# Kernel tuning notes

Measured on AMD Instinct MI355X. Metric: run time of the kernel, lower is better.

## Reference

```python
import jax, jax.numpy as jnp
import numpy as np

N, E, R = 50000, 500000, 3
IN, HID, OUT = 128, 128, 128
NEG_SLOPE = 0.2


def setup_inputs() -> dict:
    key = jax.random.key(0)
    ks = jax.random.split(key, 16)
    g = lambda i, shape: jax.random.normal(ks[i], shape, jnp.float32) * 0.1
    return {
        "x": jax.random.normal(ks[0], (N, IN), jnp.float32),
        "edge_index": jax.random.randint(ks[1], (2, E), 0, N, jnp.int32),
        "edge_type": jax.random.randint(ks[2], (E,), 0, R, jnp.int32),
        "edge_attr": jax.random.normal(ks[3], (E, 1), jnp.float32),
        # conv1 params (RGATConv: per-relation weight, q/k/e attention vectors, edge lin, bias)
        "w1": g(4, (R, IN, HID)), "q1": g(5, (HID, 1)), "k1": g(6, (HID, 1)),
        "le1": g(7, (1, HID)), "e1": g(8, (HID, 1)), "b1": jnp.zeros((HID,), jnp.float32),
        # conv2 params
        "w2": g(9, (R, HID, OUT)), "q2": g(10, (OUT, 1)), "k2": g(11, (OUT, 1)),
        "le2": g(12, (1, OUT)), "e2": g(13, (OUT, 1)), "b2": jnp.zeros((OUT,), jnp.float32),
    }


def _rgat_conv(x, src, dst, edge_type, edge_attr, w, q, k, le, e, b):
    """PyG RGATConv: heads=1, dim=1, additive-self-attention, across-relation softmax."""
    n = x.shape[0]
    # Per-relation linear at node level (equiv. to per-edge bmm with w[edge_type])
    xw = jnp.einsum('ni,rio->rno', x, w)            # [R, N, C]
    x_j = xw[edge_type, src]                          # [E, C] transformed source feats
    x_i = xw[edge_type, dst]                          # [E, C] transformed target feats
    # additive attention logits: q(x_i) + k(x_j) + e(lin_edge(edge_attr))
    alpha = x_i @ q + x_j @ k + (edge_attr @ le) @ e  # [E, 1]
    alpha = jax.nn.leaky_relu(alpha, negative_slope=NEG_SLOPE)
    # across-relation softmax over incoming edges of each target node
    amax = jax.ops.segment_max(alpha, dst, num_segments=n)
    amax = jnp.where(jnp.isfinite(amax), amax, 0.0)   # empty segments -> 0
    ex = jnp.exp(alpha - amax[dst])
    denom = jax.ops.segment_sum(ex, dst, num_segments=n)
    alpha = ex / (denom[dst] + 1e-16)
    # weighted scatter-add aggregation, then bias (concat=True, heads=1)
    out = jax.ops.segment_sum(alpha * x_j, dst, num_segments=n)  # [N, C]
    return out + b


def reference(x, edge_index, edge_type, edge_attr,
              w1, q1, k1, le1, e1, b1,
              w2, q2, k2, le2, e2, b2):
    src, dst = edge_index[0], edge_index[1]
    h = jax.nn.relu(_rgat_conv(x, src, dst, edge_type, edge_attr, w1, q1, k1, le1, e1, b1))
    return _rgat_conv(h, src, dst, edge_type, edge_attr, w2, q2, k2, le2, e2, b2)
```

## Files before the change

kernel.cpp:

```cpp
#include <hip/hip_runtime.h>
#include <hip/hip_bf16.h>
#include <math.h>

typedef __bf16 bf16x8 __attribute__((ext_vector_type(8)));
typedef float f32x4 __attribute__((ext_vector_type(4)));

#define CDIM 128

__global__ void sentinel_kernel(float* outf) {
  if (threadIdx.x == 0) outf[0] = 12345.0f;
}

__global__ __launch_bounds__(256) void prep_kernel(
    const float* __restrict__ w1, const float* __restrict__ w2,
    __hip_bfloat16* __restrict__ wt,
    const float* __restrict__ le1, const float* __restrict__ e1,
    const float* __restrict__ le2, const float* __restrict__ e2,
    float* __restrict__ outc, int* __restrict__ deg, int perW, int n) {
  const int b = blockIdx.x;
  const int tid = threadIdx.x;
  if (b < 48) {
    int t = b * 256 + tid;
    if (t >= perW * 2) return;
    const float* w = (t < perW) ? w1 : w2;
    int tt = (t < perW) ? t : t - perW;
    int r = tt >> 11;
    int rem = tt & 2047;
    int kb = rem >> 7;
    int o = rem & 127;
    const float* wr = w + ((size_t)r << 14);
    union { __hip_bfloat16 h[8]; int4 v; } u;
#pragma unroll
    for (int j = 0; j < 8; ++j)
      u.h[j] = __float2bfloat16(wr[(size_t)(kb * 8 + j) * CDIM + o]);
    *reinterpret_cast<int4*>(wt + (size_t)t * 8) = u.v;
  } else if (b == 48) {
    __shared__ float s1[128], s2[128];
    int t = tid;
    if (t < 128) { s1[t] = le1[t] * e1[t]; s2[t] = le2[t] * e2[t]; }
    __syncthreads();
    for (int off = 64; off > 0; off >>= 1) {
      if (t < off) { s1[t] += s1[t + off]; s2[t] += s2[t + off]; }
      __syncthreads();
    }
    if (t == 0) { outc[0] = s1[0]; outc[1] = s2[0]; }
  } else {
    int i = (b - 49) * 256 + tid;
    if (i < n) deg[i] = 0;
  }
}


__global__ __launch_bounds__(256) void hist_kernel(const int* __restrict__ dstv,
                                                   int* __restrict__ deg, int E) {
  int e = blockIdx.x * 256 + threadIdx.x;
  if (e < E) atomicAdd(&deg[dstv[e]], 1);
}

__global__ __launch_bounds__(256) void scan1_kernel(const int* __restrict__ deg,
                                                    int* __restrict__ rowptr,
                                                    int* __restrict__ partials, int n) {
  __shared__ int sh[256];
  int t = threadIdx.x;
  int base = blockIdx.x * 1024;
  int idx = base + t * 4;
  int v[4]; int s = 0;
#pragma unroll
  for (int j = 0; j < 4; ++j) { v[j] = (idx + j < n) ? deg[idx + j] : 0; s += v[j]; }
  sh[t] = s;
  __syncthreads();
  for (int off = 1; off < 256; off <<= 1) {
    int x = (t >= off) ? sh[t - off] : 0;
    __syncthreads();
    sh[t] += x;
    __syncthreads();
  }
  int excl = sh[t] - s;
  if (t == 255) partials[blockIdx.x] = sh[255];
  int run = excl;
#pragma unroll
  for (int j = 0; j < 4; ++j) {
    if (idx + j < n) rowptr[idx + j] = run;
    run += v[j];
  }
}

__global__ __launch_bounds__(256) void scan2_kernel(int* __restrict__ partials, int nb) {
  __shared__ int sh[256];
  int carry = 0;
  for (int base = 0; base < nb; base += 256) {
    int i = base + threadIdx.x;
    int v = (i < nb) ? partials[i] : 0;
    sh[threadIdx.x] = v;
    __syncthreads();
    for (int off = 1; off < 256; off <<= 1) {
      int x = (threadIdx.x >= off) ? sh[threadIdx.x - off] : 0;
      __syncthreads();
      sh[threadIdx.x] += x;
      __syncthreads();
    }
    if (i < nb) partials[i] = carry + sh[threadIdx.x] - v;
    carry += sh[255];
    __syncthreads();
  }
}

__global__ __launch_bounds__(256) void scan3_kernel(int* __restrict__ rowptr,
                                                    int* __restrict__ cursor,
                                                    const int* __restrict__ partials,
                                                    int n, int E) {
  int i = blockIdx.x * 256 + threadIdx.x;
  if (i < n) {
    int v = rowptr[i] + partials[i >> 10];
    rowptr[i] = v;
    cursor[i] = v;
  } else if (i == n) {
    rowptr[n] = E;
  }
}

__global__ __launch_bounds__(256) void scatter_kernel(
    const int* __restrict__ srcv, const int* __restrict__ dstv,
    const int* __restrict__ etype, const float* __restrict__ eattr,
    int* __restrict__ cursor, int2* __restrict__ kattr, int E, int n) {
  int e = blockIdx.x * 256 + threadIdx.x;
  if (e >= E) return;
  int p = atomicAdd(&cursor[dstv[e]], 1);
  kattr[p] = make_int2(etype[e] * n + srcv[e], __float_as_int(eattr[e]));
}

__global__ __launch_bounds__(256) void gemm_xw_kernel(
    const float* __restrict__ xin, const __hip_bfloat16* __restrict__ wt,
    const float* __restrict__ qv, const float* __restrict__ kv,
    __hip_bfloat16* __restrict__ xwout, float* __restrict__ sq, float* __restrict__ sk,
    int n) {
  __shared__ __hip_bfloat16 wlds[16 * 128 * 8];
  const int r = blockIdx.y;
  const int base = blockIdx.x * 128;
  const int tid = threadIdx.x;
  {
    const int4* src = reinterpret_cast<const int4*>(wt + ((size_t)r << 14));
    int4* dst = reinterpret_cast<int4*>(wlds);
    for (int i = tid; i < 2048; i += 256) dst[i] = src[i];
  }
  __syncthreads();

  const int wave = tid >> 6, lane = tid & 63;
  const int quad = lane >> 4, c16 = lane & 15;

  bf16x8 zf;
#pragma unroll
  for (int j = 0; j < 8; ++j) zf[j] = (__bf16)0.0f;

  bf16x8 af[2][4];
#pragma unroll
  for (int h = 0; h < 2; ++h) {
    int m = base + wave * 32 + h * 16 + c16;
#pragma unroll
    for (int ks = 0; ks < 4; ++ks) {
      if (m < n) {
        const float* xp = xin + (size_t)m * CDIM + ks * 32 + quad * 8;
        f32x4 x0 = *reinterpret_cast<const f32x4*>(xp);
        f32x4 x1 = *reinterpret_cast<const f32x4*>(xp + 4);
        bf16x8 a;
#pragma unroll
        for (int j = 0; j < 4; ++j) { a[j] = (__bf16)x0[j]; a[4 + j] = (__bf16)x1[j]; }
        af[h][ks] = a;
      } else {
        af[h][ks] = zf;
      }
    }
  }

  f32x4 acc[2][8];
#pragma unroll
  for (int h = 0; h < 2; ++h)
#pragma unroll
    for (int nt = 0; nt < 8; ++nt) acc[h][nt] = (f32x4){0.f, 0.f, 0.f, 0.f};

#pragma unroll
  for (int ks = 0; ks < 4; ++ks) {
#pragma unroll
    for (int nt = 0; nt < 8; ++nt) {
      bf16x8 b = *reinterpret_cast<const bf16x8*>(
          &wlds[(((ks * 4 + quad) * 128) + nt * 16 + c16) * 8]);
      acc[0][nt] = __builtin_amdgcn_mfma_f32_16x16x32_bf16(af[0][ks], b, acc[0][nt], 0, 0, 0);
      acc[1][nt] = __builtin_amdgcn_mfma_f32_16x16x32_bf16(af[1][ks], b, acc[1][nt], 0, 0, 0);
    }
  }

  float qf[8], kf[8];
#pragma unroll
  for (int nt = 0; nt < 8; ++nt) {
    qf[nt] = qv[nt * 16 + c16];
    kf[nt] = kv[nt * 16 + c16];
  }

#pragma unroll
  for (int h = 0; h < 2; ++h) {
    int rowb = base + wave * 32 + h * 16 + quad * 4;
#pragma unroll
    for (int reg = 0; reg < 4; ++reg) {
      int grow = rowb + reg;
      float s_q = 0.f, s_k = 0.f;
#pragma unroll
      for (int nt = 0; nt < 8; ++nt) {
        float v = acc[h][nt][reg];
        if (grow < n)
          xwout[(((size_t)r * n + grow) << 7) + nt * 16 + c16] = __float2bfloat16(v);
        s_q += v * qf[nt];
        s_k += v * kf[nt];
      }
#pragma unroll
      for (int off = 1; off < 16; off <<= 1) {
        s_q += __shfl_xor(s_q, off, 64);
        s_k += __shfl_xor(s_k, off, 64);
      }
      if (c16 == 0 && grow < n) {
        sq[r * n + grow] = s_q;
        sk[r * n + grow] = s_k;
      }
    }
  }
}

__global__ __launch_bounds__(256) void aggregate_kernel(
    const int* __restrict__ rowptr, const int2* __restrict__ kattr,
    const float* __restrict__ sq, const float* __restrict__ sk,
    const __hip_bfloat16* __restrict__ xw, const float* __restrict__ bias,
    const float* __restrict__ cscal, float* __restrict__ out, int n, int do_relu) {
  const int wave = threadIdx.x >> 6, lane = threadIdx.x & 63;
  const int node = blockIdx.x * 4 + wave;
  if (node >= n) return;
  const int g = lane >> 4;
  const int sub = lane & 15;
  const float c = cscal[0];
  const int n2 = n * 2;

  const int start = rowptr[node];
  const int deg = rowptr[node + 1] - start;
  const float s0 = sq[node], s1 = sq[n + node], s2 = sq[n2 + node];

  float acc[8];
#pragma unroll
  for (int t = 0; t < 8; ++t) acc[t] = 0.f;
  float den = 0.f;

  for (int j0 = 0; j0 < deg; j0 += 4) {
    int j = j0 + g;
    if (j < deg) {
      int2 ka = kattr[start + j];
      int kk = ka.x;
      float sv = (kk >= n2) ? s2 : ((kk >= n) ? s1 : s0);
      float l = sv + sk[kk] + c * __int_as_float(ka.y);
      l = l > 0.f ? l : 0.2f * l;
      float w = __expf(l);
      bf16x8 f = *reinterpret_cast<const bf16x8*>(xw + ((size_t)kk << 7) + sub * 8);
#pragma unroll
      for (int t = 0; t < 8; ++t) acc[t] += w * (float)f[t];
      den += w;
    }
  }

#pragma unroll
  for (int t = 0; t < 8; ++t) {
    acc[t] += __shfl_xor(acc[t], 16, 64);
    acc[t] += __shfl_xor(acc[t], 32, 64);
  }
  den += __shfl_xor(den, 16, 64);
  den += __shfl_xor(den, 32, 64);

  if (g == 0) {
    float inv = 1.0f / (den + 1e-16f);
    f32x4 b0 = *reinterpret_cast<const f32x4*>(bias + sub * 8);
    f32x4 b1 = *reinterpret_cast<const f32x4*>(bias + sub * 8 + 4);
    f32x4 o0, o1;
#pragma unroll
    for (int t = 0; t < 4; ++t) {
      o0[t] = acc[t] * inv + b0[t];
      o1[t] = acc[4 + t] * inv + b1[t];
    }
    if (do_relu) {
#pragma unroll
      for (int t = 0; t < 4; ++t) {
        o0[t] = fmaxf(o0[t], 0.f);
        o1[t] = fmaxf(o1[t], 0.f);
      }
    }
    float* op = out + (size_t)node * CDIM + sub * 8;
    *reinterpret_cast<f32x4*>(op) = o0;
    *reinterpret_cast<f32x4*>(op + 4) = o1;
  }
}


extern "C" void kernel_launch(void* const* d_in, const int* in_sizes, int n_in,
                              void* d_out, int out_size, void* d_ws, size_t ws_size,
                              hipStream_t stream) {
  const float* x     = (const float*)d_in[0];
  const int*   eidx  = (const int*)d_in[1];
  const int*   etype = (const int*)d_in[2];
  const float* eattr = (const float*)d_in[3];
  const float* w1  = (const float*)d_in[4];
  const float* q1  = (const float*)d_in[5];
  const float* k1  = (const float*)d_in[6];
  const float* le1 = (const float*)d_in[7];
  const float* e1  = (const float*)d_in[8];
  const float* b1  = (const float*)d_in[9];
  const float* w2  = (const float*)d_in[10];
  const float* q2  = (const float*)d_in[11];
  const float* k2  = (const float*)d_in[12];
  const float* le2 = (const float*)d_in[13];
  const float* e2  = (const float*)d_in[14];
  const float* b2  = (const float*)d_in[15];

  const int N = in_sizes[0] / CDIM;
  const int E = in_sizes[2];
  const int R = in_sizes[4] / (CDIM * CDIM);
  const int* srcv = eidx;
  const int* dstv = eidx + E;

  char* p = (char*)d_ws;
  auto alloc = [&](size_t bytes) -> void* {
    void* q = (void*)p;
    p += (bytes + 255) & ~(size_t)255;
    return q;
  };
  float* sq       = (float*)alloc((size_t)R * N * 4);
  float* sk       = (float*)alloc((size_t)R * N * 4);
  int*   deg      = (int*)alloc((size_t)N * 4);
  int*   rowptr   = (int*)alloc((size_t)(N + 1) * 4);
  int*   cursor   = (int*)alloc((size_t)N * 4);
  int*   partials = (int*)alloc(4096);
  int2*  kattr    = (int2*)alloc((size_t)E * 8);
  __hip_bfloat16* wt = (__hip_bfloat16*)alloc((size_t)2 * R * CDIM * CDIM * 2);
  float* cscal    = (float*)alloc(256);
  __hip_bfloat16* xw = (__hip_bfloat16*)alloc((size_t)R * N * CDIM * 2);

  size_t needed = (size_t)(p - (char*)d_ws);
  if (needed > ws_size) {
    sentinel_kernel<<<1, 64, 0, stream>>>((float*)d_out);
    return;
  }

  float* outp = (float*)d_out;
  float* hbuf = outp;

  const int eg = (E + 255) / 256;
  const int nb = (N + 1023) / 1024;
  const int nodes4 = (N + 3) / 4;
  const int perW = R * 2048;
  const int prep_grid = 49 + (N + 255) / 256;

  prep_kernel<<<prep_grid, 256, 0, stream>>>(w1, w2, wt, le1, e1, le2, e2,
                                             cscal, deg, perW, N);

  hist_kernel<<<eg, 256, 0, stream>>>(dstv, deg, E);
  scan1_kernel<<<nb, 256, 0, stream>>>(deg, rowptr, partials, N);
  scan2_kernel<<<1, 256, 0, stream>>>(partials, nb);
  scan3_kernel<<<(N + 1 + 255) / 256, 256, 0, stream>>>(rowptr, cursor, partials, N, E);
  scatter_kernel<<<eg, 256, 0, stream>>>(srcv, dstv, etype, eattr, cursor, kattr, E, N);

  dim3 ggrid((N + 127) / 128, R);

  gemm_xw_kernel<<<ggrid, 256, 0, stream>>>(x, wt, q1, k1, xw, sq, sk, N);
  aggregate_kernel<<<nodes4, 256, 0, stream>>>(rowptr, kattr, sq, sk, xw, b1,
                                               cscal + 0, hbuf, N, 1);

  gemm_xw_kernel<<<ggrid, 256, 0, stream>>>(hbuf, wt + (size_t)R * CDIM * CDIM,
                                            q2, k2, xw, sq, sk, N);
  aggregate_kernel<<<nodes4, 256, 0, stream>>>(rowptr, kattr, sq, sk, xw, b2,
                                               cscal + 1, outp, N, 0);
}
```

Measured before the change: 274.5 us.

## Fuse CSR build into one cooperative kernel and loop relations inside GEMM

The six preprocessing kernels (weight convert, degree histogram, three-phase scan, scatter) are merged into a single cooperative-launch kernel separated by grid-wide syncs, removing launch gaps between them. The GEMM kernel now loops over the three relations inside each block, loading each relation's weights into LDS in turn and reusing the converted x fragments, instead of using a 2D grid with one relation per block. Risks include grid.sync overhead, a single-block partials scan that assumes nb<=256, and reduced GEMM parallelism since there are a third as many blocks.

```diff
diff --git a/kernel.cpp b/kernel.cpp
--- a/kernel.cpp
+++ b/kernel.cpp
@@ -1,6 +1,9 @@
 #include <hip/hip_runtime.h>
 #include <hip/hip_bf16.h>
+#include <hip/hip_cooperative_groups.h>
 #include <math.h>
+
+namespace cg = cooperative_groups;
 
 typedef __bf16 bf16x8 __attribute__((ext_vector_type(8)));
 typedef float f32x4 __attribute__((ext_vector_type(4)));
@@ -11,17 +14,23 @@
   if (threadIdx.x == 0) outf[0] = 12345.0f;
 }
 
-__global__ __launch_bounds__(256) void prep_kernel(
+__global__ __launch_bounds__(256) void build_kernel(
     const float* __restrict__ w1, const float* __restrict__ w2,
     __hip_bfloat16* __restrict__ wt,
     const float* __restrict__ le1, const float* __restrict__ e1,
     const float* __restrict__ le2, const float* __restrict__ e2,
-    float* __restrict__ outc, int* __restrict__ deg, int perW, int n) {
-  const int b = blockIdx.x;
-  const int tid = threadIdx.x;
-  if (b < 48) {
-    int t = b * 256 + tid;
-    if (t >= perW * 2) return;
+    float* __restrict__ cscal, int* __restrict__ deg,
+    const int* __restrict__ srcv, const int* __restrict__ dstv,
+    const int* __restrict__ etype, const float* __restrict__ eattr,
+    int* __restrict__ rowptr, int* __restrict__ cursor,
+    int* __restrict__ partials, int2* __restrict__ kattr,
+    int perW, int n, int E, int nb) {
+  cg::grid_group grid = cg::this_grid();
+  __shared__ int sh[256];
+  const int gsize = gridDim.x * 256;
+  const int gtid = blockIdx.x * 256 + threadIdx.x;
+
+  for (int t = gtid; t < perW * 2; t += gsize) {
     const float* w = (t < perW) ? w1 : w2;
     int tt = (t < perW) ? t : t - perW;
     int r = tt >> 11;
@@ -34,99 +43,81 @@
     for (int j = 0; j < 8; ++j)
       u.h[j] = __float2bfloat16(wr[(size_t)(kb * 8 + j) * CDIM + o]);
     *reinterpret_cast<int4*>(wt + (size_t)t * 8) = u.v;
-  } else if (b == 48) {
-    __shared__ float s1[128], s2[128];
-    int t = tid;
-    if (t < 128) { s1[t] = le1[t] * e1[t]; s2[t] = le2[t] * e2[t]; }
-    __syncthreads();
-    for (int off = 64; off > 0; off >>= 1) {
-      if (t < off) { s1[t] += s1[t + off]; s2[t] += s2[t + off]; }
-      __syncthreads();
-    }
-    if (t == 0) { outc[0] = s1[0]; outc[1] = s2[0]; }
-  } else {
-    int i = (b - 49) * 256 + tid;
-    if (i < n) deg[i] = 0;
-  }
-}
-
-
-__global__ __launch_bounds__(256) void hist_kernel(const int* __restrict__ dstv,
-                                                   int* __restrict__ deg, int E) {
-  int e = blockIdx.x * 256 + threadIdx.x;
-  if (e < E) atomicAdd(&deg[dstv[e]], 1);
-}
-
-__global__ __launch_bounds__(256) void scan1_kernel(const int* __restrict__ deg,
-                                                    int* __restrict__ rowptr,
-                                                    int* __restrict__ partials, int n) {
-  __shared__ int sh[256];
-  int t = threadIdx.x;
-  int base = blockIdx.x * 1024;
-  int idx = base + t * 4;
-  int v[4]; int s = 0;
-#pragma unroll
-  for (int j = 0; j < 4; ++j) { v[j] = (idx + j < n) ? deg[idx + j] : 0; s += v[j]; }
-  sh[t] = s;
-  __syncthreads();
-  for (int off = 1; off < 256; off <<= 1) {
-    int x = (t >= off) ? sh[t - off] : 0;
-    __syncthreads();
-    sh[t] += x;
-    __syncthreads();
-  }
-  int excl = sh[t] - s;
-  if (t == 255) partials[blockIdx.x] = sh[255];
-  int run = excl;
-#pragma unroll
-  for (int j = 0; j < 4; ++j) {
-    if (idx + j < n) rowptr[idx + j] = run;
-    run += v[j];
-  }
-}
-
-__global__ __launch_bounds__(256) void scan2_kernel(int* __restrict__ partials, int nb) {
-  __shared__ int sh[256];
-  int carry = 0;
-  for (int base = 0; base < nb; base += 256) {
-    int i = base + threadIdx.x;
-    int v = (i < nb) ? partials[i] : 0;
-    sh[threadIdx.x] = v;
+  }
+  if (blockIdx.x == 0 && threadIdx.x < 64) {
+    int t = threadIdx.x;
+    float v1 = le1[t] * e1[t] + le1[t + 64] * e1[t + 64];
+    float v2 = le2[t] * e2[t] + le2[t + 64] * e2[t + 64];
+#pragma unroll
+    for (int off = 32; off > 0; off >>= 1) {
+      v1 += __shfl_xor(v1, off, 64);
+      v2 += __shfl_xor(v2, off, 64);
+    }
+    if (t == 0) { cscal[0] = v1; cscal[1] = v2; }
+  }
+  for (int i = gtid; i < n; i += gsize) deg[i] = 0;
+  grid.sync();
+
+  for (int e = gtid; e < E; e += gsize) atomicAdd(&deg[dstv[e]], 1);
+  grid.sync();
+
+  for (int chunk = blockIdx.x; chunk < nb; chunk += gridDim.x) {
+    int t = threadIdx.x;
+    int base = chunk * 1024;
+    int idx = base + t * 4;
+    int v[4]; int s = 0;
+#pragma unroll
+    for (int j = 0; j < 4; ++j) { v[j] = (idx + j < n) ? deg[idx + j] : 0; s += v[j]; }
+    sh[t] = s;
     __syncthreads();
     for (int off = 1; off < 256; off <<= 1) {
-      int x = (threadIdx.x >= off) ? sh[threadIdx.x - off] : 0;
+      int x = (t >= off) ? sh[t - off] : 0;
       __syncthreads();
-      sh[threadIdx.x] += x;
+      sh[t] += x;
       __syncthreads();
     }
-    if (i < nb) partials[i] = carry + sh[threadIdx.x] - v;
-    carry += sh[255];
+    int excl = sh[t] - s;
+    if (t == 255) partials[chunk] = sh[255];
+    int run = excl;
+#pragma unroll
+    for (int j = 0; j < 4; ++j) {
+      if (idx + j < n) rowptr[idx + j] = run;
+      run += v[j];
+    }
     __syncthreads();
   }
-}
-
-__global__ __launch_bounds__(256) void scan3_kernel(int* __restrict__ rowptr,
-                                                    int* __restrict__ cursor,
-                                                    const int* __restrict__ partials,
-                                                    int n, int E) {
-  int i = blockIdx.x * 256 + threadIdx.x;
-  if (i < n) {
-    int v = rowptr[i] + partials[i >> 10];
-    rowptr[i] = v;
-    cursor[i] = v;
-  } else if (i == n) {
-    rowptr[n] = E;
-  }
-}
-
-__global__ __launch_bounds__(256) void scatter_kernel(
-    const int* __restrict__ srcv, const int* __restrict__ dstv,
-    const int* __restrict__ etype, const float* __restrict__ eattr,
-    int* __restrict__ cursor, int2* __restrict__ kattr, int E, int n) {
-  int e = blockIdx.x * 256 + threadIdx.x;
-  if (e >= E) return;
-  int p = atomicAdd(&cursor[dstv[e]], 1);
-  kattr[p] = make_int2(etype[e] * n + srcv[e], __float_as_int(eattr[e]));
+  grid.sync();
+
+  if (blockIdx.x == 0) {
+    int t = threadIdx.x;
+    int v = (t < nb) ? partials[t] : 0;
+    sh[t] = v;
+    __syncthreads();
+    for (int off = 1; off < 256; off <<= 1) {
+      int x = (t >= off) ? sh[t - off] : 0;
+      __syncthreads();
+      sh[t] += x;
+      __syncthreads();
+    }
+    if (t < nb) partials[t] = sh[t] - v;
+  }
+  grid.sync();
+
+  for (int i = gtid; i <= n; i += gsize) {
+    if (i < n) {
+      int v = rowptr[i] + partials[i >> 10];
+      rowptr[i] = v;
+      cursor[i] = v;
+    } else {
+      rowptr[n] = E;
+    }
+  }
+  grid.sync();
+
+  for (int e = gtid; e < E; e += gsize) {
+    int p = atomicAdd(&cursor[dstv[e]], 1);
+    kattr[p] = make_int2(etype[e] * n + srcv[e], __float_as_int(eattr[e]));
+  }
 }
 
 __global__ __launch_bounds__(256) void gemm_xw_kernel(
@@ -135,16 +126,8 @@
     __hip_bfloat16* __restrict__ xwout, float* __restrict__ sq, float* __restrict__ sk,
     int n) {
   __shared__ __hip_bfloat16 wlds[16 * 128 * 8];
-  const int r = blockIdx.y;
   const int base = blockIdx.x * 128;
   const int tid = threadIdx.x;
-  {
-    const int4* src = reinterpret_cast<const int4*>(wt + ((size_t)r << 14));
-    int4* dst = reinterpret_cast<int4*>(wlds);
-    for (int i = tid; i < 2048; i += 256) dst[i] = src[i];
-  }
-  __syncthreads();
-
   const int wave = tid >> 6, lane = tid & 63;
   const int quad = lane >> 4, c16 = lane & 15;
 
@@ -172,23 +155,6 @@
     }
   }
 
-  f32x4 acc[2][8];
-#pragma unroll
-  for (int h = 0; h < 2; ++h)
-#pragma unroll
-    for (int nt = 0; nt < 8; ++nt) acc[h][nt] = (f32x4){0.f, 0.f, 0.f, 0.f};
-
-#pragma unroll
-  for (int ks = 0; ks < 4; ++ks) {
-#pragma unroll
-    for (int nt = 0; nt < 8; ++nt) {
-      bf16x8 b = *reinterpret_cast<const bf16x8*>(
-          &wlds[(((ks * 4 + quad) * 128) + nt * 16 + c16) * 8]);
-      acc[0][nt] = __builtin_amdgcn_mfma_f32_16x16x32_bf16(af[0][ks], b, acc[0][nt], 0, 0, 0);
-      acc[1][nt] = __builtin_amdgcn_mfma_f32_16x16x32_bf16(af[1][ks], b, acc[1][nt], 0, 0, 0);
-    }
-  }
-
   float qf[8], kf[8];
 #pragma unroll
   for (int nt = 0; nt < 8; ++nt) {
@@ -196,29 +162,56 @@
     kf[nt] = kv[nt * 16 + c16];
   }
 
-#pragma unroll
-  for (int h = 0; h < 2; ++h) {
-    int rowb = base + wave * 32 + h * 16 + quad * 4;
-#pragma unroll
-    for (int reg = 0; reg < 4; ++reg) {
-      int grow = rowb + reg;
-      float s_q = 0.f, s_k = 0.f;
+  for (int r = 0; r < 3; ++r) {
+    if (r) __syncthreads();
+    {
+      const int4* src = reinterpret_cast<const int4*>(wt + ((size_t)r << 14));
+      int4* dst = reinterpret_cast<int4*>(wlds);
+      for (int i = tid; i < 2048; i += 256) dst[i] = src[i];
+    }
+    __syncthreads();
+
+    f32x4 acc[2][8];
+#pragma unroll
+    for (int h = 0; h < 2; ++h)
+#pragma unroll
+      for (int nt = 0; nt < 8; ++nt) acc[h][nt] = (f32x4){0.f, 0.f, 0.f, 0.f};
+
+#pragma unroll
+    for (int ks = 0; ks < 4; ++ks) {
 #pragma unroll
       for (int nt = 0; nt < 8; ++nt) {
-        float v = acc[h][nt][reg];
-        if (grow < n)
-          xwout[(((size_t)r * n + grow) << 7) + nt * 16 + c16] = __float2bfloat16(v);
-        s_q += v * qf[nt];
-        s_k += v * kf[nt];
+        bf16x8 b = *reinterpret_cast<const bf16x8*>(
+            &wlds[(((ks * 4 + quad) * 128) + nt * 16 + c16) * 8]);
+        acc[0][nt] = __builtin_amdgcn_mfma_f32_16x16x32_bf16(af[0][ks], b, acc[0][nt], 0, 0, 0);
+        acc[1][nt] = __builtin_amdgcn_mfma_f32_16x16x32_bf16(af[1][ks], b, acc[1][nt], 0, 0, 0);
       }
-#pragma unroll
-      for (int off = 1; off < 16; off <<= 1) {
-        s_q += __shfl_xor(s_q, off, 64);
-        s_k += __shfl_xor(s_k, off, 64);
-      }
-      if (c16 == 0 && grow < n) {
-        sq[r * n + grow] = s_q;
-        sk[r * n + grow] = s_k;
+    }
+
+#pragma unroll
+    for (int h = 0; h < 2; ++h) {
+      int rowb = base + wave * 32 + h * 16 + quad * 4;
+#pragma unroll
+      for (int reg = 0; reg < 4; ++reg) {
+        int grow = rowb + reg;
+        float s_q = 0.f, s_k = 0.f;
+#pragma unroll
+        for (int nt = 0; nt < 8; ++nt) {
+          float v = acc[h][nt][reg];
+          if (grow < n)
+            xwout[(((size_t)r * n + grow) << 7) + nt * 16 + c16] = __float2bfloat16(v);
+          s_q += v * qf[nt];
+          s_k += v * kf[nt];
+        }
+#pragma unroll
+        for (int off = 1; off < 16; off <<= 1) {
+          s_q += __shfl_xor(s_q, off, 64);
+          s_k += __shfl_xor(s_k, off, 64);
+        }
+        if (c16 == 0 && grow < n) {
+          sq[r * n + grow] = s_q;
+          sk[r * n + grow] = s_k;
+        }
       }
     }
   }
@@ -346,22 +339,24 @@
   float* outp = (float*)d_out;
   float* hbuf = outp;
 
-  const int eg = (E + 255) / 256;
   const int nb = (N + 1023) / 1024;
   const int nodes4 = (N + 3) / 4;
-  const int perW = R * 2048;
-  const int prep_grid = 49 + (N + 255) / 256;
-
-  prep_kernel<<<prep_grid, 256, 0, stream>>>(w1, w2, wt, le1, e1, le2, e2,
-                                             cscal, deg, perW, N);
-
-  hist_kernel<<<eg, 256, 0, stream>>>(dstv, deg, E);
-  scan1_kernel<<<nb, 256, 0, stream>>>(deg, rowptr, partials, N);
-  scan2_kernel<<<1, 256, 0, stream>>>(partials, nb);
-  scan3_kernel<<<(N + 1 + 255) / 256, 256, 0, stream>>>(rowptr, cursor, partials, N, E);
-  scatter_kernel<<<eg, 256, 0, stream>>>(srcv, dstv, etype, eattr, cursor, kattr, E, N);
-
-  dim3 ggrid((N + 127) / 128, R);
+  int perW = R * 2048;
+
+  {
+    int nI = N, eI = E, nbI = nb;
+    void* args[] = {
+        (void*)&w1, (void*)&w2, (void*)&wt,
+        (void*)&le1, (void*)&e1, (void*)&le2, (void*)&e2,
+        (void*)&cscal, (void*)&deg,
+        (void*)&srcv, (void*)&dstv, (void*)&etype, (void*)&eattr,
+        (void*)&rowptr, (void*)&cursor, (void*)&partials, (void*)&kattr,
+        (void*)&perW, (void*)&nI, (void*)&eI, (void*)&nbI};
+    hipLaunchCooperativeKernel((const void*)build_kernel, dim3(1024), dim3(256),
+                               args, 0, stream);
+  }
+
+  dim3 ggrid((N + 127) / 128);
 
   gemm_xw_kernel<<<ggrid, 256, 0, stream>>>(x, wt, q1, k1, xw, sq, sk, N);
   aggregate_kernel<<<nodes4, 256, 0, stream>>>(rowptr, kattr, sq, sk, xw, b1,
```

New measurement: 756.3 us. 2.76x slower.
